# Kernel optimization log

Hardware: AMD Instinct MI355X
Metric: run time of the kernel (lower is better)

Reference implementation:

```python
import jax, jax.numpy as jnp
import numpy as np

N, E, H, C, NG = 50000, 800000, 4, 64, 32
HC = H * C  # 256


def setup_inputs() -> dict:
    key = jax.random.key(0)
    ks = jax.random.split(key, 32)
    f32 = jnp.float32
    def rn(k, shape, s=0.1):
        return jax.random.normal(k, shape, dtype=f32) * s
    inp = {}
    inp['x'] = jax.random.normal(ks[0], (N, 4), dtype=f32)
    inp['edge_index'] = jax.random.randint(ks[1], (2, E), 0, N, dtype=jnp.int32)
    inp['edge_attr'] = jax.random.normal(ks[2], (E, 1), dtype=f32)
    inp['batch'] = jnp.sort(jax.random.randint(ks[3], (N,), 0, NG, dtype=jnp.int32))
    # encoder
    inp['enc_w'] = rn(ks[4], (4, 64)); inp['enc_b'] = rn(ks[5], (64,))
    # GATv2 layer 1: in 64 -> H*C (lin_l source, lin_r target, lin_edge, att, bias)
    inp['g1_wl'] = rn(ks[6], (64, HC)); inp['g1_bl'] = rn(ks[7], (HC,))
    inp['g1_wr'] = rn(ks[8], (64, HC)); inp['g1_br'] = rn(ks[9], (HC,))
    inp['g1_we'] = rn(ks[10], (1, HC))
    inp['g1_att'] = rn(ks[11], (H, C))
    inp['g1_bias'] = rn(ks[12], (HC,))
    # GATv2 layer 2: in 256 -> H*C
    inp['g2_wl'] = rn(ks[13], (HC, HC)); inp['g2_bl'] = rn(ks[14], (HC,))
    inp['g2_wr'] = rn(ks[15], (HC, HC)); inp['g2_br'] = rn(ks[16], (HC,))
    inp['g2_we'] = rn(ks[17], (1, HC))
    inp['g2_att'] = rn(ks[18], (H, C))
    inp['g2_bias'] = rn(ks[19], (HC,))
    # post MLP: 256 -> 128 (LayerNorm, ReLU) -> 64 (ReLU)
    inp['p1_w'] = rn(ks[20], (HC, 128)); inp['p1_b'] = rn(ks[21], (128,))
    inp['ln_g'] = jnp.ones((128,), dtype=f32); inp['ln_b'] = jnp.zeros((128,), dtype=f32)
    inp['p2_w'] = rn(ks[22], (128, 64)); inp['p2_b'] = rn(ks[23], (64,))
    return inp


def _gatv2_layer(x, src, dst, eattr, wl, bl, wr, br, we, att, bias):
    # PyG GATv2Conv: alpha_e = att . leaky_relu(lin_l(x_src) + lin_r(x_dst) + lin_edge(e))
    n = x.shape[0]
    xl = (x @ wl + bl).reshape(n, H, C)   # source-side messages
    xr = (x @ wr + br).reshape(n, H, C)   # target-side
    e = (eattr @ we).reshape(-1, H, C)
    m = jax.nn.leaky_relu(xl[src] + xr[dst] + e, 0.2)        # [E',H,C]
    alpha = jnp.einsum('ehc,hc->eh', m, att)                  # [E',H]
    amax = jax.lax.stop_gradient(jax.ops.segment_max(alpha, dst, num_segments=n))
    ex = jnp.exp(alpha - amax[dst])
    den = jax.ops.segment_sum(ex, dst, num_segments=n)
    a = ex / den[dst]                                          # softmax per dst node
    out = jax.ops.segment_sum(a[:, :, None] * xl[src], dst, num_segments=n)
    return out.reshape(n, HC) + bias


def reference(x, edge_index, edge_attr, batch, enc_w, enc_b,
              g1_wl, g1_bl, g1_wr, g1_br, g1_we, g1_att, g1_bias,
              g2_wl, g2_bl, g2_wr, g2_br, g2_we, g2_att, g2_bias,
              p1_w, p1_b, ln_g, ln_b, p2_w, p2_b):
    n = x.shape[0]
    src0, dst0 = edge_index[0], edge_index[1]
    # PyG default add_self_loops=True with fill_value='mean' for edge_attr
    deg = jnp.maximum(jax.ops.segment_sum(jnp.ones_like(edge_attr[:, 0]), dst0, num_segments=n), 1.0)
    loop_attr = jax.ops.segment_sum(edge_attr, dst0, num_segments=n) / deg[:, None]
    idx = jnp.arange(n, dtype=src0.dtype)
    src = jnp.concatenate([src0, idx]); dst = jnp.concatenate([dst0, idx])
    eattr = jnp.concatenate([edge_attr, loop_attr], axis=0)
    h = jax.nn.relu(x @ enc_w + enc_b)
    h = jax.nn.relu(_gatv2_layer(h, src, dst, eattr, g1_wl, g1_bl, g1_wr, g1_br, g1_we, g1_att, g1_bias))
    h = jax.nn.relu(_gatv2_layer(h, src, dst, eattr, g2_wl, g2_bl, g2_wr, g2_br, g2_we, g2_att, g2_bias))
    # global mean pool over graphs
    cnt = jnp.maximum(jax.ops.segment_sum(jnp.ones((n,), h.dtype), batch, num_segments=NG), 1.0)
    g = jax.ops.segment_sum(h, batch, num_segments=NG) / cnt[:, None]
    # post MLP (dropout is identity in eval)
    z = g @ p1_w + p1_b
    mu = jnp.mean(z, axis=-1, keepdims=True)
    var = jnp.mean((z - mu) ** 2, axis=-1, keepdims=True)
    z = (z - mu) / jnp.sqrt(var + 1e-5) * ln_g + ln_b
    z = jax.nn.relu(z)
    z = jax.nn.relu(z @ p2_w + p2_b)
    return z
```

## Files before the change

### kernel.cpp

```cpp
#include <hip/hip_runtime.h>

#define CDIV(a,b) (((a)+(b)-1)/(b))

typedef __bf16 bf16_t;
typedef unsigned char u8;
typedef bf16_t bf16x8 __attribute__((ext_vector_type(8)));
typedef bf16_t bf16x4 __attribute__((ext_vector_type(4)));
typedef float floatx4 __attribute__((ext_vector_type(4)));
typedef float floatx2 __attribute__((ext_vector_type(2)));

__device__ __forceinline__ int sigma2(int p) {
    int tile = p >> 7, hh = (p >> 6) & 1, m = (p >> 2) & 15, c = p & 3;
    return tile * 128 + (hh * 4 + c) * 16 + m;
}

__device__ __forceinline__ unsigned pack4_fp8(float a, float b, float c, float d) {
    int v = __builtin_amdgcn_cvt_pk_fp8_f32(a, b, 0, false);
    v = __builtin_amdgcn_cvt_pk_fp8_f32(c, d, v, true);
    return (unsigned)v;
}

template<bool HI>
__device__ __forceinline__ floatx2 cvtf8(unsigned v) {
    return __builtin_amdgcn_cvt_pk_f32_fp8(v, HI);
}

__global__ void k_deg(const int* __restrict__ ei, const float* __restrict__ ea,
                      int* __restrict__ deg, float* __restrict__ lsum, int E) {
    int e = blockIdx.x * 256 + threadIdx.x;
    if (e >= E) return;
    int d = ei[E + e];
    atomicAdd(&deg[d], 1);
    atomicAdd(&lsum[d], ea[e]);
}

__global__ void k_scanA(const int* __restrict__ deg, int* __restrict__ part, int n) {
    __shared__ int sh[256];
    int t = threadIdx.x;
    int i = blockIdx.x * 256 + t;
    int v = (i < n) ? deg[i] + 1 : 0;
    sh[t] = v;
    __syncthreads();
    for (int d = 128; d > 0; d >>= 1) { if (t < d) sh[t] += sh[t + d]; __syncthreads(); }
    if (t == 0) part[blockIdx.x] = sh[0];
}
__global__ void k_scanB(int* __restrict__ part, int nb) {
    __shared__ int sh[256];
    int t = threadIdx.x;
    int v = (t < nb) ? part[t] : 0;
    sh[t] = v;
    __syncthreads();
    for (int d = 1; d < 256; d <<= 1) {
        int u = (t >= d) ? sh[t - d] : 0;
        __syncthreads();
        sh[t] += u;
        __syncthreads();
    }
    if (t < nb) part[t] = sh[t] - v;
}
__global__ void k_scanC(const int* __restrict__ deg, const int* __restrict__ part,
                        int* __restrict__ off, float* __restrict__ lsum, int n) {
    __shared__ int sh[256];
    int t = threadIdx.x;
    int i = blockIdx.x * 256 + t;
    int dv = (i < n) ? deg[i] : 0;
    int v = (i < n) ? dv + 1 : 0;
    sh[t] = v;
    __syncthreads();
    for (int d = 1; d < 256; d <<= 1) {
        int u = (t >= d) ? sh[t - d] : 0;
        __syncthreads();
        sh[t] += u;
        __syncthreads();
    }
    int excl = part[blockIdx.x] + sh[t] - v;
    if (i < n) {
        off[i] = excl;
        lsum[i] = lsum[i] / fmaxf((float)dv, 1.0f);
    }
    if (i == n - 1) off[n] = excl + v;
}

__global__ void k_fill(const int* __restrict__ ei, const float* __restrict__ ea,
                       const float* __restrict__ lattr, const int* __restrict__ off,
                       int* __restrict__ cursor, int2* __restrict__ csr, int E, int n) {
    int e = blockIdx.x * 256 + threadIdx.x;
    int EE = E + n;
    if (e >= EE) return;
    int s, d; float a;
    if (e < E) { s = ei[e]; d = ei[E + e]; a = ea[e]; }
    else       { s = e - E; d = s;         a = lattr[s]; }
    int pos = off[d] + atomicAdd(&cursor[d], 1);
    csr[pos] = make_int2(s, __float_as_int(a));
}

__global__ void k_wcast2(const float* __restrict__ Wl, const float* __restrict__ Wr,
                         const float* __restrict__ bl, const float* __restrict__ br,
                         bf16_t* __restrict__ Wt, float* __restrict__ bias2,
                         int K, int kshift, int permK,
                         const float* __restrict__ we, const float* __restrict__ att,
                         const float* __restrict__ cb,
                         float* __restrict__ wep, float* __restrict__ attp,
                         float* __restrict__ cbp) {
    int idx = blockIdx.x * 256 + threadIdx.x;
    if (idx < 512) bias2[idx] = (idx < 256) ? bl[idx] : br[idx - 256];
    if (idx < 256) {
        int sg = sigma2(idx);
        wep[idx] = we[sg]; attp[idx] = att[sg]; cbp[idx] = cb[sg];
    }
    if (idx >= 512 * K) return;
    int nn = idx >> kshift, k = idx & (K - 1);
    int ks = permK ? sigma2(k) : k;
    float v = (nn < 256) ? Wl[ks * 256 + nn] : Wr[ks * 256 + (nn - 256)];
    Wt[idx] = (bf16_t)v;
}

__global__ __launch_bounds__(256) void k_gemm1_fused(
        const float* __restrict__ x, const float* __restrict__ encw,
        const float* __restrict__ encb, const bf16_t* __restrict__ Wt,
        const float* __restrict__ bias2, u8* __restrict__ XL,
        u8* __restrict__ XR, int nrows) {
    __shared__ bf16_t As[128 * 32];
    __shared__ bf16_t Bs[128 * 32];
    int tid = threadIdx.x;
    int w = tid >> 6, lane = tid & 63;
    int quad = lane >> 4, m = lane & 15;
    int row0 = blockIdx.x * 128;
    int ct0 = blockIdx.y * 2;
    bf16x8 afr[2][2];
    floatx4 acc[2][8];

    for (int ctile = ct0; ctile < ct0 + 2; ++ctile) {
        int n0 = ctile * 128;
#pragma unroll
        for (int rt = 0; rt < 2; ++rt)
#pragma unroll
            for (int ct = 0; ct < 8; ++ct)
                acc[rt][ct] = (floatx4){0.f, 0.f, 0.f, 0.f};
        for (int k0c = 0; k0c < 2; ++k0c) {
            __syncthreads();
            if (ctile == ct0) {
#pragma unroll
                for (int i = 0; i < 2; ++i) {
                    int c = tid + i * 256;
                    int r = c >> 2, kc = c & 3;
                    int sw = (kc + (r >> 1)) & 3;
                    int gr = row0 + r; if (gr >= nrows) gr = nrows - 1;
                    float4 xv = ((const float4*)x)[gr];
                    bf16x8 v;
#pragma unroll
                    for (int kk = 0; kk < 8; ++kk) {
                        int k = k0c * 32 + kc * 8 + kk;
                        float s = encb[k];
                        s = fmaf(xv.x, encw[k], s);
                        s = fmaf(xv.y, encw[64 + k], s);
                        s = fmaf(xv.z, encw[128 + k], s);
                        s = fmaf(xv.w, encw[192 + k], s);
                        v[kk] = (bf16_t)fmaxf(s, 0.0f);
                    }
                    *(bf16x8*)&As[r * 32 + sw * 8] = v;
                }
            }
#pragma unroll
            for (int i = 0; i < 2; ++i) {
                int c = tid + i * 256;
                int r = c >> 2, kc = c & 3;
                int sw = (kc + (r >> 1)) & 3;
                bf16x8 v = *(const bf16x8*)&Wt[(size_t)(n0 + r) * 64 + k0c * 32 + kc * 8];
                *(bf16x8*)&Bs[r * 32 + sw * 8] = v;
            }
            __syncthreads();
            if (ctile == ct0) {
#pragma unroll
                for (int rt = 0; rt < 2; ++rt) {
                    int ar = w * 32 + rt * 16 + m;
                    afr[k0c][rt] = *(bf16x8*)&As[ar * 32 + (((quad + (ar >> 1)) & 3) * 8)];
                }
            }
            bf16x8 bfr[8];
#pragma unroll
            for (int ct = 0; ct < 8; ++ct) {
                int br = ct * 16 + m;
                bfr[ct] = *(bf16x8*)&Bs[br * 32 + (((quad + (br >> 1)) & 3) * 8)];
            }
#pragma unroll
            for (int ct = 0; ct < 8; ++ct) {
                acc[0][ct] = __builtin_amdgcn_mfma_f32_16x16x32_bf16(afr[k0c][0], bfr[ct], acc[0][ct], 0, 0, 0);
                acc[1][ct] = __builtin_amdgcn_mfma_f32_16x16x32_bf16(afr[k0c][1], bfr[ct], acc[1][ct], 0, 0, 0);
            }
        }
        int tile = ctile & 1;
        u8* dst = (ctile < 2) ? XL : XR;
        float bv[8];
#pragma unroll
        for (int ct = 0; ct < 8; ++ct) bv[ct] = bias2[n0 + ct * 16 + m];
#pragma unroll
        for (int rt = 0; rt < 2; ++rt) {
#pragma unroll
            for (int i = 0; i < 4; ++i) {
                int row = row0 + w * 32 + rt * 16 + quad * 4 + i;
                if (row < nrows) {
                    unsigned w0 = pack4_fp8(acc[rt][0][i] + bv[0], acc[rt][1][i] + bv[1],
                                            acc[rt][2][i] + bv[2], acc[rt][3][i] + bv[3]);
                    unsigned w1 = pack4_fp8(acc[rt][4][i] + bv[4], acc[rt][5][i] + bv[5],
                                            acc[rt][6][i] + bv[6], acc[rt][7][i] + bv[7]);
                    *(unsigned*)&dst[(size_t)row * 256 + tile * 128 + m * 4] = w0;
                    *(unsigned*)&dst[(size_t)row * 256 + tile * 128 + 64 + m * 4] = w1;
                }
            }
        }
    }
}

__global__ __launch_bounds__(256) void k_gemm2(
        const bf16_t* __restrict__ Hb, const bf16_t* __restrict__ Wt,
        const float* __restrict__ bias2, u8* __restrict__ XL,
        u8* __restrict__ XR, int nrows) {
    const int K = 256;
    __shared__ bf16_t As[128 * 32];
    __shared__ bf16_t Bs[128 * 32];
    int tid = threadIdx.x;
    int w = tid >> 6, lane = tid & 63;
    int quad = lane >> 4, m = lane & 15;
    int row0 = blockIdx.x * 128;
    int ct0 = blockIdx.y * 2;
    bf16x8 afr[8][2];
    floatx4 acc[2][8];

    for (int ctile = ct0; ctile < ct0 + 2; ++ctile) {
        int n0 = ctile * 128;
#pragma unroll
        for (int rt = 0; rt < 2; ++rt)
#pragma unroll
            for (int ct = 0; ct < 8; ++ct)
                acc[rt][ct] = (floatx4){0.f, 0.f, 0.f, 0.f};
        for (int k0c = 0; k0c < 8; ++k0c) {
            __syncthreads();
            if (ctile == ct0) {
#pragma unroll
                for (int i = 0; i < 2; ++i) {
                    int c = tid + i * 256;
                    int r = c >> 2, kc = c & 3;
                    int sw = (kc + (r >> 1)) & 3;
                    int gr = row0 + r; if (gr >= nrows) gr = nrows - 1;
                    bf16x8 v = *(const bf16x8*)&Hb[(size_t)gr * K + k0c * 32 + kc * 8];
                    *(bf16x8*)&As[r * 32 + sw * 8] = v;
                }
            }
#pragma unroll
            for (int i = 0; i < 2; ++i) {
                int c = tid + i * 256;
                int r = c >> 2, kc = c & 3;
                int sw = (kc + (r >> 1)) & 3;
                bf16x8 v = *(const bf16x8*)&Wt[(size_t)(n0 + r) * K + k0c * 32 + kc * 8];
                *(bf16x8*)&Bs[r * 32 + sw * 8] = v;
            }
            __syncthreads();
            if (ctile == ct0) {
#pragma unroll
                for (int rt = 0; rt < 2; ++rt) {
                    int ar = w * 32 + rt * 16 + m;
                    afr[k0c][rt] = *(bf16x8*)&As[ar * 32 + (((quad + (ar >> 1)) & 3) * 8)];
                }
            }
            bf16x8 bfr[8];
#pragma unroll
            for (int ct = 0; ct < 8; ++ct) {
                int br = ct * 16 + m;
                bfr[ct] = *(bf16x8*)&Bs[br * 32 + (((quad + (br >> 1)) & 3) * 8)];
            }
#pragma unroll
            for (int ct = 0; ct < 8; ++ct) {
                acc[0][ct] = __builtin_amdgcn_mfma_f32_16x16x32_bf16(afr[k0c][0], bfr[ct], acc[0][ct], 0, 0, 0);
                acc[1][ct] = __builtin_amdgcn_mfma_f32_16x16x32_bf16(afr[k0c][1], bfr[ct], acc[1][ct], 0, 0, 0);
            }
        }
        int tile = ctile & 1;
        u8* dst = (ctile < 2) ? XL : XR;
        float bv[8];
#pragma unroll
        for (int ct = 0; ct < 8; ++ct) bv[ct] = bias2[n0 + ct * 16 + m];
#pragma unroll
        for (int rt = 0; rt < 2; ++rt) {
#pragma unroll
            for (int i = 0; i < 4; ++i) {
                int row = row0 + w * 32 + rt * 16 + quad * 4 + i;
                if (row < nrows) {
                    unsigned w0 = pack4_fp8(acc[rt][0][i] + bv[0], acc[rt][1][i] + bv[1],
                                            acc[rt][2][i] + bv[2], acc[rt][3][i] + bv[3]);
                    unsigned w1 = pack4_fp8(acc[rt][4][i] + bv[4], acc[rt][5][i] + bv[5],
                                            acc[rt][6][i] + bv[6], acc[rt][7][i] + bv[7]);
                    *(unsigned*)&dst[(size_t)row * 256 + tile * 128 + m * 4] = w0;
                    *(unsigned*)&dst[(size_t)row * 256 + tile * 128 + 64 + m * 4] = w1;
                }
            }
        }
    }
}

__device__ __forceinline__ void pair_step(
        int p, int p1, int half, int loff,
        const int2* __restrict__ csr, const u8* __restrict__ XL,
        floatx2 xr01, floatx2 xr23, floatx2 xr45, floatx2 xr67,
        floatx2 wv01, floatx2 wv23, floatx2 wv45, floatx2 wv67,
        floatx2 av01, floatx2 av23, floatx2 av45, floatx2 av67,
        float& s, floatx2& a01, floatx2& a23, floatx2& a45, floatx2& a67) {
    int idx = p + half;
    bool valid = idx < p1;
    int idc = valid ? idx : p1 - 1;
    int2 ed = csr[idc];
    int src = ed.x;
    float eav = __int_as_float(ed.y);
    uint2 u = *(const uint2*)(XL + (size_t)src * 256 + loff);
    floatx2 x01 = cvtf8<false>(u.x);
    floatx2 x23 = cvtf8<true>(u.x);
    floatx2 x45 = cvtf8<false>(u.y);
    floatx2 x67 = cvtf8<true>(u.y);
    floatx2 t01 = x01 + xr01 + eav * wv01;
    floatx2 t23 = x23 + xr23 + eav * wv23;
    floatx2 t45 = x45 + xr45 + eav * wv45;
    floatx2 t67 = x67 + xr67 + eav * wv67;
    t01 = __builtin_elementwise_max(t01, 0.2f * t01);
    t23 = __builtin_elementwise_max(t23, 0.2f * t23);
    t45 = __builtin_elementwise_max(t45, 0.2f * t45);
    t67 = __builtin_elementwise_max(t67, 0.2f * t67);
    floatx2 d = t01 * av01 + t23 * av23 + t45 * av45 + t67 * av67;
    float al = d.x + d.y;
    al += __shfl_xor(al, 1);
    al += __shfl_xor(al, 2);
    al += __shfl_xor(al, 4);
    float wg = valid ? exp2f(al) : 0.0f;
    s += wg;
    a01 += wg * x01; a23 += wg * x23; a45 += wg * x45; a67 += wg * x67;
}

__global__ void k_conv(
                       const u8* __restrict__ XL, const u8* __restrict__ XR,
                       const float* __restrict__ wep, const float* __restrict__ attp,
                       const int2* __restrict__ csr,
                       const int* __restrict__ off, const float* __restrict__ cbp,
                       bf16_t* __restrict__ outb, int n) {
    int wid = (blockIdx.x * 256 + threadIdx.x) >> 6;
    int lane = threadIdx.x & 63;
    if (wid >= n) return;
    int l = lane & 31, half = lane >> 5;
    int loff = l * 8;
    uint2 ur = *(const uint2*)(XR + (size_t)wid * 256 + loff);
    floatx2 xr01 = cvtf8<false>(ur.x);
    floatx2 xr23 = cvtf8<true>(ur.x);
    floatx2 xr45 = cvtf8<false>(ur.y);
    floatx2 xr67 = cvtf8<true>(ur.y);
    float4 wa = ((const float4*)wep)[2 * l], wb = ((const float4*)wep)[2 * l + 1];
    float4 aa = ((const float4*)attp)[2 * l], ab = ((const float4*)attp)[2 * l + 1];
    floatx2 wv01 = {wa.x, wa.y}, wv23 = {wa.z, wa.w};
    floatx2 wv45 = {wb.x, wb.y}, wv67 = {wb.z, wb.w};
    const float LOG2E = 1.44269504f;
    floatx2 av01 = {aa.x * LOG2E, aa.y * LOG2E}, av23 = {aa.z * LOG2E, aa.w * LOG2E};
    floatx2 av45 = {ab.x * LOG2E, ab.y * LOG2E}, av67 = {ab.z * LOG2E, ab.w * LOG2E};
    int p0 = off[wid], p1 = off[wid + 1];
    float s = 0.f;
    floatx2 a01 = {0.f, 0.f}, a23 = {0.f, 0.f}, a45 = {0.f, 0.f}, a67 = {0.f, 0.f};
    int p = p0;
    for (; p + 4 <= p1; p += 4) {
        pair_step(p,     p1, half, loff, csr, XL, xr01, xr23, xr45, xr67,
                  wv01, wv23, wv45, wv67, av01, av23, av45, av67, s, a01, a23, a45, a67);
        pair_step(p + 2, p1, half, loff, csr, XL, xr01, xr23, xr45, xr67,
                  wv01, wv23, wv45, wv67, av01, av23, av45, av67, s, a01, a23, a45, a67);
    }
    for (; p < p1; p += 2)
        pair_step(p,     p1, half, loff, csr, XL, xr01, xr23, xr45, xr67,
                  wv01, wv23, wv45, wv67, av01, av23, av45, av67, s, a01, a23, a45, a67);
    s += __shfl_xor(s, 32);
    a01.x += __shfl_xor(a01.x, 32); a01.y += __shfl_xor(a01.y, 32);
    a23.x += __shfl_xor(a23.x, 32); a23.y += __shfl_xor(a23.y, 32);
    a45.x += __shfl_xor(a45.x, 32); a45.y += __shfl_xor(a45.y, 32);
    a67.x += __shfl_xor(a67.x, 32); a67.y += __shfl_xor(a67.y, 32);
    if (half == 0) {
        float inv = 1.0f / s;
        float4 ba = ((const float4*)cbp)[2 * l], bb = ((const float4*)cbp)[2 * l + 1];
        bf16x8 ob;
        ob[0] = (bf16_t)fmaxf(fmaf(a01.x, inv, ba.x), 0.f);
        ob[1] = (bf16_t)fmaxf(fmaf(a01.y, inv, ba.y), 0.f);
        ob[2] = (bf16_t)fmaxf(fmaf(a23.x, inv, ba.z), 0.f);
        ob[3] = (bf16_t)fmaxf(fmaf(a23.y, inv, ba.w), 0.f);
        ob[4] = (bf16_t)fmaxf(fmaf(a45.x, inv, bb.x), 0.f);
        ob[5] = (bf16_t)fmaxf(fmaf(a45.y, inv, bb.y), 0.f);
        ob[6] = (bf16_t)fmaxf(fmaf(a67.x, inv, bb.z), 0.f);
        ob[7] = (bf16_t)fmaxf(fmaf(a67.y, inv, bb.w), 0.f);
        *(bf16x8*)&outb[(size_t)wid * 256 + l * 8] = ob;
    }
}

__global__ void k_pool(const bf16_t* __restrict__ h, const int* __restrict__ batch,
                       float* __restrict__ gsum, float* __restrict__ gcnt, int n) {
    int j = threadIdx.x;
    int start = blockIdx.x * 32;
    if (start >= n) return;
    int end = start + 32; if (end > n) end = n;
    int cur = batch[start];
    float acc = 0.0f, cnt = 0.0f;
    for (int i = start; i < end; ++i) {
        int g = batch[i];
        if (g != cur) {
            atomicAdd(&gsum[cur * 256 + j], acc);
            if (j == 0) atomicAdd(&gcnt[cur], cnt);
            acc = 0.0f; cnt = 0.0f; cur = g;
        }
        acc += (float)h[(size_t)i * 256 + j];
        cnt += 1.0f;
    }
    atomicAdd(&gsum[cur * 256 + j], acc);
    if (j == 0) atomicAdd(&gcnt[cur], cnt);
}

__global__ void k_mlp(const float* __restrict__ gsum, const float* __restrict__ gcnt,
                      const float* __restrict__ p1w, const float* __restrict__ p1b,
                      const float* __restrict__ lng, const float* __restrict__ lnb,
                      const float* __restrict__ p2w, const float* __restrict__ p2b,
                      float* __restrict__ out) {
    int g = blockIdx.x;
    int t = threadIdx.x;
    __shared__ float gv[256];
    __shared__ float z[128];
    __shared__ float red[128];
    float invc = 1.0f / fmaxf(gcnt[g], 1.0f);
    gv[sigma2(t)]       = gsum[g * 256 + t] * invc;
    gv[sigma2(t + 128)] = gsum[g * 256 + 128 + t] * invc;
    __syncthreads();
    float z1 = p1b[t];
    for (int k = 0; k < 256; ++k) z1 = fmaf(gv[k], p1w[k * 128 + t], z1);
    red[t] = z1;
    __syncthreads();
    for (int d = 64; d > 0; d >>= 1) { if (t < d) red[t] += red[t + d]; __syncthreads(); }
    float mu = red[0] * (1.0f / 128.0f);
    __syncthreads();
    float dz = z1 - mu;
    red[t] = dz * dz;
    __syncthreads();
    for (int d = 64; d > 0; d >>= 1) { if (t < d) red[t] += red[t + d]; __syncthreads(); }
    float var = red[0] * (1.0f / 128.0f);
    float zn = dz * rsqrtf(var + 1e-5f) * lng[t] + lnb[t];
    z[t] = fmaxf(zn, 0.0f);
    __syncthreads();
    if (t < 64) {
        float o = p2b[t];
        for (int k = 0; k < 128; ++k) o = fmaf(z[k], p2w[k * 64 + t], o);
        out[g * 64 + t] = fmaxf(o, 0.0f);
    }
}

extern "C" void kernel_launch(void* const* d_in, const int* in_sizes, int n_in,
                              void* d_out, int out_size, void* d_ws, size_t ws_size,
                              hipStream_t stream) {
    const float* x      = (const float*)d_in[0];
    const int*   ei     = (const int*)d_in[1];
    const float* ea     = (const float*)d_in[2];
    const int*   batch  = (const int*)d_in[3];
    const float* enc_w  = (const float*)d_in[4];
    const float* enc_b  = (const float*)d_in[5];
    const float* g1_wl  = (const float*)d_in[6];
    const float* g1_bl  = (const float*)d_in[7];
    const float* g1_wr  = (const float*)d_in[8];
    const float* g1_br  = (const float*)d_in[9];
    const float* g1_we  = (const float*)d_in[10];
    const float* g1_att = (const float*)d_in[11];
    const float* g1_bias= (const float*)d_in[12];
    const float* g2_wl  = (const float*)d_in[13];
    const float* g2_bl  = (const float*)d_in[14];
    const float* g2_wr  = (const float*)d_in[15];
    const float* g2_br  = (const float*)d_in[16];
    const float* g2_we  = (const float*)d_in[17];
    const float* g2_att = (const float*)d_in[18];
    const float* g2_bias= (const float*)d_in[19];
    const float* p1_w   = (const float*)d_in[20];
    const float* p1_b   = (const float*)d_in[21];
    const float* ln_g   = (const float*)d_in[22];
    const float* ln_b   = (const float*)d_in[23];
    const float* p2_w   = (const float*)d_in[24];
    const float* p2_b   = (const float*)d_in[25];
    float* out = (float*)d_out;

    const int N  = in_sizes[3];
    const int E  = in_sizes[1] / 2;
    const int EE = E + N;
    const int NB = CDIV(N, 256);

    u8*     XL  = (u8*)d_ws;
    u8*     XR  = XL + (size_t)N * 256;
    bf16_t* Hb  = (bf16_t*)(XR + (size_t)N * 256);
    bf16_t* Wt  = Hb + (size_t)N * 256;
    int2*  csr  = (int2*)(Wt + 512 * 256);
    float* lsum  = (float*)(csr + EE);
    float* gsum  = lsum + N;
    float* gcnt  = gsum + 32 * 256;
    int*   deg   = (int*)(gcnt + 32);
    int*   cursor= deg + N;
    float* bias2 = (float*)(cursor + N);
    float* wep   = bias2 + 512;
    float* attp  = wep + 256;
    float* cbp   = attp + 256;
    int*   part  = (int*)(cbp + 256);
    int*   off   = part + 256;

    (void)hipMemsetAsync(lsum, 0, (size_t)(3 * N + 32 * 256 + 32) * sizeof(float), stream);

    k_deg<<<CDIV(E, 256), 256, 0, stream>>>(ei, ea, deg, lsum, E);
    k_scanA<<<NB, 256, 0, stream>>>(deg, part, N);
    k_scanB<<<1, 256, 0, stream>>>(part, NB);
    k_scanC<<<NB, 256, 0, stream>>>(deg, part, off, lsum, N);
    k_fill<<<CDIV(EE, 256), 256, 0, stream>>>(ei, ea, lsum, off, cursor, csr, E, N);

    dim3 ggrid(CDIV(N, 128), 2);

    k_wcast2<<<CDIV(512 * 64, 256), 256, 0, stream>>>(g1_wl, g1_wr, g1_bl, g1_br, Wt, bias2,
                                                      64, 6, 0, g1_we, g1_att, g1_bias,
                                                      wep, attp, cbp);
    k_gemm1_fused<<<ggrid, 256, 0, stream>>>(x, enc_w, enc_b, Wt, bias2, XL, XR, N);
    k_conv<<<CDIV(N, 4), 256, 0, stream>>>(XL, XR, wep, attp, csr, off, cbp, Hb, N);

    k_wcast2<<<CDIV(512 * 256, 256), 256, 0, stream>>>(g2_wl, g2_wr, g2_bl, g2_br, Wt, bias2,
                                                       256, 8, 1, g2_we, g2_att, g2_bias,
                                                       wep, attp, cbp);
    k_gemm2<<<ggrid, 256, 0, stream>>>(Hb, Wt, bias2, XL, XR, N);
    k_conv<<<CDIV(N, 4), 256, 0, stream>>>(XL, XR, wep, attp, csr, off, cbp, Hb, N);

    k_pool<<<CDIV(N, 32), 256, 0, stream>>>(Hb, batch, gsum, gcnt, N);
    k_mlp<<<32, 128, 0, stream>>>(gsum, gcnt, p1_w, p1_b, ln_g, ln_b, p2_w, p2_b, out);
}
```

Before: 465.8 us.

## Compute self-loop attrs from CSR instead of float atomics; nontemporal conv loads/stores

Drops the per-edge float atomicAdd of edge attributes in k_deg. The self-loop mean attribute is now computed by a new k_selfloop kernel that walks each node's CSR segment after fill and writes the self-loop entry into the last slot. The conv kernel also reads CSR entries with nontemporal loads and writes its output with nontemporal stores, to reduce cache pollution. This adds one kernel launch and a serial per-node loop over incoming edges, and the floating-point summation order changes.

Result: no change. 465.3 us (-0.1%).

```diff
diff --git a/kernel.cpp b/kernel.cpp
--- a/kernel.cpp
+++ b/kernel.cpp
@@ -5,9 +5,9 @@
 typedef __bf16 bf16_t;
 typedef unsigned char u8;
 typedef bf16_t bf16x8 __attribute__((ext_vector_type(8)));
-typedef bf16_t bf16x4 __attribute__((ext_vector_type(4)));
 typedef float floatx4 __attribute__((ext_vector_type(4)));
 typedef float floatx2 __attribute__((ext_vector_type(2)));
+typedef unsigned uintx4 __attribute__((ext_vector_type(4)));
 
 __device__ __forceinline__ int sigma2(int p) {
     int tile = p >> 7, hh = (p >> 6) & 1, m = (p >> 2) & 15, c = p & 3;
@@ -25,13 +25,10 @@
     return __builtin_amdgcn_cvt_pk_f32_fp8(v, HI);
 }
 
-__global__ void k_deg(const int* __restrict__ ei, const float* __restrict__ ea,
-                      int* __restrict__ deg, float* __restrict__ lsum, int E) {
+__global__ void k_deg(const int* __restrict__ ei, int* __restrict__ deg, int E) {
     int e = blockIdx.x * 256 + threadIdx.x;
     if (e >= E) return;
-    int d = ei[E + e];
-    atomicAdd(&deg[d], 1);
-    atomicAdd(&lsum[d], ea[e]);
+    atomicAdd(&deg[ei[E + e]], 1);
 }
 
 __global__ void k_scanA(const int* __restrict__ deg, int* __restrict__ part, int n) {
@@ -59,12 +56,11 @@
     if (t < nb) part[t] = sh[t] - v;
 }
 __global__ void k_scanC(const int* __restrict__ deg, const int* __restrict__ part,
-                        int* __restrict__ off, float* __restrict__ lsum, int n) {
+                        int* __restrict__ off, int n) {
     __shared__ int sh[256];
     int t = threadIdx.x;
     int i = blockIdx.x * 256 + t;
-    int dv = (i < n) ? deg[i] : 0;
-    int v = (i < n) ? dv + 1 : 0;
+    int v = (i < n) ? deg[i] + 1 : 0;
     sh[t] = v;
     __syncthreads();
     for (int d = 1; d < 256; d <<= 1) {
@@ -74,24 +70,28 @@
         __syncthreads();
     }
     int excl = part[blockIdx.x] + sh[t] - v;
-    if (i < n) {
-        off[i] = excl;
-        lsum[i] = lsum[i] / fmaxf((float)dv, 1.0f);
-    }
+    if (i < n) off[i] = excl;
     if (i == n - 1) off[n] = excl + v;
 }
 
 __global__ void k_fill(const int* __restrict__ ei, const float* __restrict__ ea,
-                       const float* __restrict__ lattr, const int* __restrict__ off,
-                       int* __restrict__ cursor, int2* __restrict__ csr, int E, int n) {
+                       const int* __restrict__ off, int* __restrict__ cursor,
+                       int2* __restrict__ csr, int E) {
     int e = blockIdx.x * 256 + threadIdx.x;
-    int EE = E + n;
-    if (e >= EE) return;
-    int s, d; float a;
-    if (e < E) { s = ei[e]; d = ei[E + e]; a = ea[e]; }
-    else       { s = e - E; d = s;         a = lattr[s]; }
+    if (e >= E) return;
+    int s = ei[e], d = ei[E + e];
     int pos = off[d] + atomicAdd(&cursor[d], 1);
-    csr[pos] = make_int2(s, __float_as_int(a));
+    csr[pos] = make_int2(s, __float_as_int(ea[e]));
+}
+
+__global__ void k_selfloop(const int* __restrict__ off, int2* __restrict__ csr, int n) {
+    int i = blockIdx.x * 256 + threadIdx.x;
+    if (i >= n) return;
+    int p0 = off[i], p1 = off[i + 1] - 1;
+    float s = 0.0f;
+    for (int p = p0; p < p1; ++p) s += __int_as_float(csr[p].y);
+    float la = s / fmaxf((float)(p1 - p0), 1.0f);
+    csr[p1] = make_int2(i, __float_as_int(la));
 }
 
 __global__ void k_wcast2(const float* __restrict__ Wl, const float* __restrict__ Wr,
@@ -308,9 +308,9 @@
     int idx = p + half;
     bool valid = idx < p1;
     int idc = valid ? idx : p1 - 1;
-    int2 ed = csr[idc];
-    int src = ed.x;
-    float eav = __int_as_float(ed.y);
+    long long ev = __builtin_nontemporal_load((const long long*)(csr + idc));
+    int src = (int)ev;
+    float eav = __int_as_float((int)(ev >> 32));
     uint2 u = *(const uint2*)(XL + (size_t)src * 256 + loff);
     floatx2 x01 = cvtf8<false>(u.x);
     floatx2 x23 = cvtf8<true>(u.x);
@@ -387,7 +387,9 @@
         ob[5] = (bf16_t)fmaxf(fmaf(a45.y, inv, bb.y), 0.f);
         ob[6] = (bf16_t)fmaxf(fmaf(a67.x, inv, bb.z), 0.f);
         ob[7] = (bf16_t)fmaxf(fmaf(a67.y, inv, bb.w), 0.f);
-        *(bf16x8*)&outb[(size_t)wid * 256 + l * 8] = ob;
+        uintx4 obits;
+        __builtin_memcpy(&obits, &ob, 16);
+        __builtin_nontemporal_store(obits, (uintx4*)&outb[(size_t)wid * 256 + l * 8]);
     }
 }
 
@@ -490,8 +492,7 @@
     bf16_t* Hb  = (bf16_t*)(XR + (size_t)N * 256);
     bf16_t* Wt  = Hb + (size_t)N * 256;
     int2*  csr  = (int2*)(Wt + 512 * 256);
-    float* lsum  = (float*)(csr + EE);
-    float* gsum  = lsum + N;
+    float* gsum  = (float*)(csr + EE);
     float* gcnt  = gsum + 32 * 256;
     int*   deg   = (int*)(gcnt + 32);
     int*   cursor= deg + N;
@@ -502,13 +503,14 @@
     int*   part  = (int*)(cbp + 256);
     int*   off   = part + 256;
 
-    (void)hipMemsetAsync(lsum, 0, (size_t)(3 * N + 32 * 256 + 32) * sizeof(float), stream);
-
-    k_deg<<<CDIV(E, 256), 256, 0, stream>>>(ei, ea, deg, lsum, E);
+    (void)hipMemsetAsync(gsum, 0, (size_t)(2 * N + 32 * 256 + 32) * sizeof(float), stream);
+
+    k_deg<<<CDIV(E, 256), 256, 0, stream>>>(ei, deg, E);
     k_scanA<<<NB, 256, 0, stream>>>(deg, part, N);
     k_scanB<<<1, 256, 0, stream>>>(part, NB);
-    k_scanC<<<NB, 256, 0, stream>>>(deg, part, off, lsum, N);
-    k_fill<<<CDIV(EE, 256), 256, 0, stream>>>(ei, ea, lsum, off, cursor, csr, E, N);
+    k_scanC<<<NB, 256, 0, stream>>>(deg, part, off, N);
+    k_fill<<<CDIV(E, 256), 256, 0, stream>>>(ei, ea, off, cursor, csr, E);
+    k_selfloop<<<NB, 256, 0, stream>>>(off, csr, N);
 
     dim3 ggrid(CDIV(N, 128), 2);
 
```
